# Kernel optimization log

Measured on AMD Instinct MI355X. Metric: run time of the kernel, lower is better.

The kernel has to match this reference:

```python
import jax, jax.numpy as jnp
import numpy as np

EPS = 1e-5
PATCH_LEN, STRIDE, SEQ_LEN = 16, 8, 512
D_FF, N_HEADS = 32, 8


def setup_inputs() -> dict:
    key = jax.random.key(0)
    ks = jax.random.split(key, 16)
    d_model, d_llm, V, num_tok, pred_len = 32, 4096, 32000, 1000, 96
    hf = N_HEADS * D_FF  # 256
    patch_nums = (SEQ_LEN - PATCH_LEN) // STRIDE + 2  # 64
    head_nf = D_FF * patch_nums  # 2048
    r = lambda k, s, fan: jax.random.normal(k, s, jnp.float32) / np.sqrt(fan)
    return {
        'x_enc': jax.random.normal(ks[0], (32, SEQ_LEN, 7), jnp.float32),
        'conv_w': r(ks[1], (d_model, PATCH_LEN, 3), PATCH_LEN * 3),
        'word_emb': jax.random.normal(ks[2], (V, d_llm), jnp.float32) * 0.02,
        'map_w': r(ks[3], (num_tok, V), V),
        'map_b': jnp.zeros((num_tok,), jnp.float32),
        'wq': r(ks[4], (hf, d_model), d_model), 'bq': jnp.zeros((hf,), jnp.float32),
        'wk': r(ks[5], (hf, d_llm), d_llm), 'bk': jnp.zeros((hf,), jnp.float32),
        'wv': r(ks[6], (hf, d_llm), d_llm), 'bv': jnp.zeros((hf,), jnp.float32),
        'wo': r(ks[7], (d_llm, hf), hf), 'bo': jnp.zeros((d_llm,), jnp.float32),
        'head_w': r(ks[8], (pred_len, head_nf), head_nf),
        'head_b': jnp.zeros((pred_len,), jnp.float32),
    }


def _forward(x_enc, conv_w, word_emb, map_w, map_b, wq, bq, wk, bk, wv, bv, wo, bo, head_w, head_b):
    B, T, N = x_enc.shape
    # RevIN normalize (stats detached, as in torch)
    mean = jax.lax.stop_gradient(jnp.mean(x_enc, axis=1, keepdims=True))
    stdev = jax.lax.stop_gradient(jnp.sqrt(jnp.var(x_enc, axis=1, keepdims=True) + EPS))
    x = (x_enc - mean) / stdev                      # [B,T,N]

    # Patch embedding: [B,N,T] -> replication pad -> unfold -> circular conv
    xt = jnp.transpose(x, (0, 2, 1))                # [B,N,T]
    xt = jnp.concatenate([xt, jnp.repeat(xt[..., -1:], STRIDE, axis=-1)], axis=-1)  # [B,N,T+stride]
    starts = jnp.arange(0, T + STRIDE - PATCH_LEN + 1, STRIDE)
    idx = starts[:, None] + jnp.arange(PATCH_LEN)   # [L, patch_len]
    patches = xt[:, :, idx]                         # [B,N,L,patch_len]
    L = patches.shape[2]
    p = patches.reshape(B * N, L, PATCH_LEN)
    # TokenEmbedding: conv1d over patch axis, circular pad 1, no bias
    pc = jnp.transpose(p, (0, 2, 1))                # [BN, patch_len, L]
    pc = jnp.concatenate([pc[..., -1:], pc, pc[..., :1]], axis=-1)
    emb = jax.lax.conv_general_dilated(pc, conv_w, (1,), 'VALID',
                                       dimension_numbers=('NCH', 'OIH', 'NCH'))
    enc = jnp.transpose(emb, (0, 2, 1))             # [BN, L, d_model]

    # Source embeddings: mapping_layer(word_emb.T).T -> [num_tokens, d_llm]
    src = (word_emb.T @ map_w.T + map_b).T          # [num_tok, d_llm]

    # Reprogramming cross-attention
    BN = enc.shape[0]
    q = (enc @ wq.T + bq).reshape(BN, L, N_HEADS, D_FF)   # [BN,L,H,E]
    k = (src @ wk.T + bk).reshape(-1, N_HEADS, D_FF)      # [S,H,E]
    v = (src @ wv.T + bv).reshape(-1, N_HEADS, D_FF)      # [S,H,E]
    scale = 1.0 / np.sqrt(D_FF)
    scores = jnp.einsum('blhe,she->bhls', q, k)
    A = jax.nn.softmax(scale * scores, axis=-1)
    rep = jnp.einsum('bhls,she->blhe', A, v).reshape(BN, L, N_HEADS * D_FF)
    out = rep @ wo.T + bo                           # [BN, L, d_llm]

    # LLM stubbed as identity; keep first d_ff channels (Time-LLM post-LLM path)
    dec = out[..., :D_FF]                           # [BN, L, d_ff]
    dec = dec.reshape(B, N, L, D_FF).transpose(0, 1, 3, 2)  # [B,N,d_ff,L]
    dec = dec.reshape(B, N, D_FF * L)               # FlattenHead
    dec = dec @ head_w.T + head_b                   # [B,N,pred_len]
    dec = jnp.transpose(dec, (0, 2, 1))             # [B,pred_len,N]
    # RevIN denormalize
    return dec * stdev + mean


def reference(x_enc, conv_w, word_emb, map_w, map_b, wq, bq, wk, bk, wv, bv, wo, bo, head_w, head_b):
    return _forward(x_enc, conv_w, word_emb, map_w, map_b, wq, bq, wk, bk, wv, bv, wo, bo, head_w, head_b)
```

## Files before the change

kernel.cpp:

```cpp
#include <hip/hip_runtime.h>
#include <math.h>

constexpr int B_ = 32, T_ = 512, N_ = 7, BN_ = 224;
constexpr int L_ = 64, DM_ = 32, PLEN_ = 16;
constexpr int HF_ = 256, NH_ = 8, DFF_ = 32;
constexpr int S_ = 1000, SP_ = 1024, DLLM_ = 4096, V_ = 32000;
constexpr int PRED_ = 96, HNF_ = 2048;
constexpr int KSPLIT2 = 25, KCH2 = 1280;

typedef short bf16x8 __attribute__((ext_vector_type(8)));
typedef float f32x4 __attribute__((ext_vector_type(4)));

__device__ inline ushort f2bf(float x) {
    union { float f; uint u; } v; v.f = x;
    uint r = v.u + 0x7fffu + ((v.u >> 16) & 1u);
    return (ushort)(r >> 16);
}
__device__ inline uint pk(float a, float b) {
    return (uint)f2bf(a) | ((uint)f2bf(b) << 16);
}
__device__ inline void gl16(const void* g, void* l) {
    __builtin_amdgcn_global_load_lds(
        (const __attribute__((address_space(1))) void*)g,
        (__attribute__((address_space(3))) void*)l, 16, 0, 0);
}

__global__ __launch_bounds__(256) void k_pre(const float* __restrict__ x,
                                             const float* __restrict__ conv_w,
                                             const float* __restrict__ wq,
                                             const float* __restrict__ bq,
                                             float* __restrict__ mean_o,
                                             float* __restrict__ std_o,
                                             float* __restrict__ qo) {
    const int bn = blockIdx.x, b = bn / N_, n = bn % N_;
    __shared__ float xn[520];
    __shared__ float cw[DM_ * PLEN_ * 3];
    __shared__ float enc_s[2048];
    __shared__ float wqs[HF_ * DM_];
    __shared__ float rs[4], rq[4], sm2[2];
    const int tid = threadIdx.x;
    const float* xp = x + (size_t)b * T_ * N_ + n;

    float s = 0.f, sq = 0.f;
    for (int t = tid; t < T_; t += 256) { float v = xp[(size_t)t * N_]; s += v; sq += v * v; }
    for (int i = tid; i < DM_ * PLEN_ * 3; i += 256) cw[i] = conv_w[i];
    for (int i = tid; i < HF_ * DM_; i += 256) wqs[i] = wq[i];
    for (int o = 32; o > 0; o >>= 1) { s += __shfl_down(s, o, 64); sq += __shfl_down(sq, o, 64); }
    int wid = tid >> 6, lane = tid & 63;
    if (lane == 0) { rs[wid] = s; rq[wid] = sq; }
    __syncthreads();
    if (tid == 0) {
        float S = rs[0] + rs[1] + rs[2] + rs[3];
        float Q = rq[0] + rq[1] + rq[2] + rq[3];
        float m = S / T_;
        float var = Q / T_ - m * m;
        float sd = sqrtf(var + 1e-5f);
        mean_o[bn] = m; std_o[bn] = sd;
        sm2[0] = m; sm2[1] = sd;
    }
    __syncthreads();
    const float m = sm2[0], rstd = 1.0f / sm2[1];
    for (int t = tid; t < T_; t += 256) xn[t] = (xp[(size_t)t * N_] - m) * rstd;
    __syncthreads();
    if (tid < 8) xn[T_ + tid] = xn[T_ - 1];
    __syncthreads();
    for (int idx = tid; idx < L_ * DM_ * 8; idx += 256) { }
    for (int idx = tid; idx < L_ * DM_; idx += 256) {
        int l = idx >> 5, o = idx & 31;
        float acc = 0.f;
        #pragma unroll
        for (int t = 0; t < 3; t++) {
            int col = l + t;
            int pcol = (col == 0) ? 63 : ((col == 65) ? 0 : col - 1);
            const float* xb = &xn[pcol * 8];
            const float* cwb = &cw[o * 48 + t];
            #pragma unroll
            for (int i = 0; i < 16; i++) acc += xb[i] * cwb[i * 3];
        }
        enc_s[idx] = acc;
    }
    __syncthreads();
    const float scale = 0.17677669529663687f;
    for (int idx = tid; idx < L_ * HF_; idx += 256) {
        int l = idx >> 8, c = idx & 255;
        float acc = bq[c];
        const float* e = &enc_s[l * 32];
        const float* w = &wqs[c * 32];
        #pragma unroll
        for (int k = 0; k < 32; k++) acc += e[k] * w[k];
        qo[(size_t)bn * L_ * HF_ + idx] = acc * scale;
    }
}

__global__ __launch_bounds__(256) void k_wsum(const float* __restrict__ wk,
                                              const float* __restrict__ wv,
                                              float* __restrict__ wsum) {
    int c = blockIdx.x;
    const float* row = (c < HF_) ? wk + (size_t)c * DLLM_ : wv + (size_t)(c - HF_) * DLLM_;
    float s = 0.f;
    for (int d = threadIdx.x; d < DLLM_; d += 256) s += row[d];
    for (int o = 32; o > 0; o >>= 1) s += __shfl_down(s, o, 64);
    __shared__ float rs[4];
    int wid = threadIdx.x >> 6, lane = threadIdx.x & 63;
    if (lane == 0) rs[wid] = s;
    __syncthreads();
    if (threadIdx.x == 0) wsum[c] = rs[0] + rs[1] + rs[2] + rs[3];
}

__global__ __launch_bounds__(256) void k_cvt_wkv(const float* __restrict__ wk,
                                                 const float* __restrict__ wv,
                                                 ushort* __restrict__ out) {
    int g = blockIdx.x * 256 + threadIdx.x;
    int e = g * 8;
    const float* src = (e < HF_ * DLLM_) ? wk + e : wv + (e - HF_ * DLLM_);
    float4 x = *(const float4*)src, y = *(const float4*)(src + 4);
    uint4 w; w.x = pk(x.x, x.y); w.y = pk(x.z, x.w); w.z = pk(y.x, y.y); w.w = pk(y.z, y.w);
    *(uint4*)(out + e) = w;
}

__global__ __launch_bounds__(512) void k_gemm1(const float* __restrict__ A,
                                               const ushort* __restrict__ Bw,
                                               ushort* __restrict__ ET) {
    __shared__ union {
        struct { float Af[2][128 * 32]; ushort Bs[2][256 * 32]; } st;
        ushort C[256 * 72];
    } lds;
    const int tid = threadIdx.x;
    const int lane = tid & 63, wid = tid >> 6;
    const int wr = wid >> 2, wc = wid & 3;
    const int n0 = blockIdx.x * 256, m0 = blockIdx.y * 128;

    const int arw = tid >> 3, acq = (tid & 7) ^ ((tid >> 3) & 7);
    const float* asrc0 = A + (size_t)(m0 + arw) * DLLM_ + acq * 4;
    const float* asrc1 = asrc0 + (size_t)64 * DLLM_;

    const int u0 = tid, rb0 = u0 >> 2, ob0 = (u0 & 3) ^ ((rb0 >> 1) & 3);
    const int u1 = tid + 512, rb1 = u1 >> 2, ob1 = (u1 & 3) ^ ((rb1 >> 1) & 3);
    const ushort* bptr0 = Bw + (size_t)(n0 + rb0) * DLLM_ + ob0 * 8;
    const ushort* bptr1 = Bw + (size_t)(n0 + rb1) * DLLM_ + ob1 * 8;

    const int rl = lane & 15, g = lane >> 4;
    const int oc = g ^ ((rl >> 1) & 3);

    f32x4 acc[4][4];
    #pragma unroll
    for (int i = 0; i < 4; i++)
        #pragma unroll
        for (int j = 0; j < 4; j++) acc[i][j] = (f32x4){0.f, 0.f, 0.f, 0.f};

    gl16(asrc0, &lds.st.Af[0][tid * 4]);
    gl16(asrc1, &lds.st.Af[0][(tid + 512) * 4]);
    gl16(bptr0, &lds.st.Bs[0][u0 * 8]);
    gl16(bptr1, &lds.st.Bs[0][u1 * 8]);
    __syncthreads();

    int cur = 0;
    constexpr int NT = DLLM_ / 32;
    for (int t = 0; t < NT; ++t) {
        if (t + 1 < NT) {
            const int o = (t + 1) * 32;
            gl16(asrc0 + o, &lds.st.Af[cur ^ 1][tid * 4]);
            gl16(asrc1 + o, &lds.st.Af[cur ^ 1][(tid + 512) * 4]);
            gl16(bptr0 + o, &lds.st.Bs[cur ^ 1][u0 * 8]);
            gl16(bptr1 + o, &lds.st.Bs[cur ^ 1][u1 * 8]);
            asm volatile("s_waitcnt vmcnt(4)" ::: "memory");
        } else {
            asm volatile("s_waitcnt vmcnt(0)" ::: "memory");
        }
        __builtin_amdgcn_s_barrier();
        asm volatile("" ::: "memory");
        const float* Ab = lds.st.Af[cur];
        const ushort* Bb = lds.st.Bs[cur];
        bf16x8 af[4], bfr[4];
        #pragma unroll
        for (int mi = 0; mi < 4; mi++) {
            int row = wr * 64 + mi * 16 + rl;
            int s = row & 7;
            int ulo = row * 8 + ((2 * g) ^ s);
            int uhi = row * 8 + ((2 * g + 1) ^ s);
            f32x4 xlo = *(const f32x4*)&Ab[ulo * 4];
            f32x4 xhi = *(const f32x4*)&Ab[uhi * 4];
            uint4 w; w.x = pk(xlo[0], xlo[1]); w.y = pk(xlo[2], xlo[3]);
            w.z = pk(xhi[0], xhi[1]); w.w = pk(xhi[2], xhi[3]);
            union { uint4 u; bf16x8 b; } cv; cv.u = w;
            af[mi] = cv.b;
        }
        #pragma unroll
        for (int ni = 0; ni < 4; ni++)
            bfr[ni] = *(const bf16x8*)&Bb[(wc * 64 + ni * 16 + rl) * 32 + oc * 8];
        __builtin_amdgcn_s_setprio(1);
        #pragma unroll
        for (int mi = 0; mi < 4; mi++)
            #pragma unroll
            for (int ni = 0; ni < 4; ni++)
                acc[mi][ni] = __builtin_amdgcn_mfma_f32_16x16x32_bf16(af[mi], bfr[ni], acc[mi][ni], 0, 0, 0);
        __builtin_amdgcn_s_setprio(0);
        asm volatile("s_waitcnt lgkmcnt(0)" ::: "memory");
        __builtin_amdgcn_s_barrier();
        cur ^= 1;
    }

    #pragma unroll
    for (int p = 0; p < 2; p++) {
        __syncthreads();
        if (wr == p) {
            #pragma unroll
            for (int mi = 0; mi < 4; mi++)
                #pragma unroll
                for (int ni = 0; ni < 4; ni++) {
                    int nl = wc * 64 + ni * 16 + (lane & 15);
                    int ml = mi * 16 + (lane >> 4) * 4;
                    uint2 w2;
                    w2.x = pk(acc[mi][ni][0], acc[mi][ni][1]);
                    w2.y = pk(acc[mi][ni][2], acc[mi][ni][3]);
                    *(uint2*)&lds.C[nl * 72 + ml] = w2;
                }
        }
        __syncthreads();
        {
            int r = tid >> 1, half = tid & 1;
            const uint4* src = (const uint4*)&lds.C[r * 72 + half * 32];
            ushort* dst = ET + (size_t)(n0 + r) * V_ + m0 + p * 64 + half * 32;
            uint4 v0 = src[0], v1 = src[1], v2 = src[2], v3 = src[3];
            *(uint4*)(dst + 0) = v0; *(uint4*)(dst + 8) = v1;
            *(uint4*)(dst + 16) = v2; *(uint4*)(dst + 24) = v3;
        }
    }
}

__global__ __launch_bounds__(256) void k_gemm2(const float* __restrict__ A,
                                               const ushort* __restrict__ ET,
                                               float* __restrict__ Cp) {
    __shared__ float Af[2][128 * 32];
    __shared__ ushort Bs[2][128 * 32];
    const int tid = threadIdx.x, lane = tid & 63, wid = tid >> 6;
    const int wr = wid >> 1, wc = wid & 1;
    const int m0 = blockIdx.x * 128, n0 = blockIdx.y * 128, kz = blockIdx.z;
    const size_t kbase = (size_t)kz * KCH2;

    const float* asrc[4];
    #pragma unroll
    for (int i = 0; i < 4; i++) {
        int u = i * 256 + tid;
        int r = u >> 3, c = (u & 7) ^ (r & 7);
        int rm = m0 + r; if (rm > S_ - 1) rm = S_ - 1;
        asrc[i] = A + (size_t)rm * V_ + kbase + c * 4;
    }
    const int u0 = tid, rb0 = u0 >> 2, ob0 = (u0 & 3) ^ ((rb0 >> 1) & 3);
    const int u1 = tid + 256, rb1 = u1 >> 2, ob1 = (u1 & 3) ^ ((rb1 >> 1) & 3);
    const ushort* bp0 = ET + (size_t)(n0 + rb0) * V_ + kbase + ob0 * 8;
    const ushort* bp1 = ET + (size_t)(n0 + rb1) * V_ + kbase + ob1 * 8;

    const int rl = lane & 15, g = lane >> 4;
    const int oB = g ^ ((rl >> 1) & 3);

    f32x4 acc[4][4];
    #pragma unroll
    for (int i = 0; i < 4; i++)
        #pragma unroll
        for (int j = 0; j < 4; j++) acc[i][j] = (f32x4){0.f, 0.f, 0.f, 0.f};

    gl16(bp0, &Bs[0][u0 * 8]);
    gl16(bp1, &Bs[0][u1 * 8]);
    #pragma unroll
    for (int i = 0; i < 4; i++) gl16(asrc[i], &Af[0][(i * 256 + tid) * 4]);
    __syncthreads();

    int cur = 0;
    constexpr int NT = KCH2 / 32;
    for (int t = 0; t < NT; ++t) {
        if (t + 1 < NT) {
            const int o = (t + 1) * 32;
            gl16(bp0 + o, &Bs[cur ^ 1][u0 * 8]);
            gl16(bp1 + o, &Bs[cur ^ 1][u1 * 8]);
            #pragma unroll
            for (int i = 0; i < 4; i++) gl16(asrc[i] + o, &Af[cur ^ 1][(i * 256 + tid) * 4]);
            asm volatile("s_waitcnt vmcnt(6)" ::: "memory");
        } else {
            asm volatile("s_waitcnt vmcnt(0)" ::: "memory");
        }
        __builtin_amdgcn_s_barrier();
        asm volatile("" ::: "memory");
        const float* Ab = Af[cur];
        const ushort* Bb = Bs[cur];
        bf16x8 af[4], bfr[4];
        #pragma unroll
        for (int mi = 0; mi < 4; mi++) {
            int row = wr * 64 + mi * 16 + rl;
            int s = row & 7;
            int ulo = row * 8 + ((2 * g) ^ s);
            int uhi = row * 8 + ((2 * g + 1) ^ s);
            f32x4 xlo = *(const f32x4*)&Ab[ulo * 4];
            f32x4 xhi = *(const f32x4*)&Ab[uhi * 4];
            uint4 w; w.x = pk(xlo[0], xlo[1]); w.y = pk(xlo[2], xlo[3]);
            w.z = pk(xhi[0], xhi[1]); w.w = pk(xhi[2], xhi[3]);
            union { uint4 u; bf16x8 b; } cv; cv.u = w;
            af[mi] = cv.b;
        }
        #pragma unroll
        for (int ni = 0; ni < 4; ni++)
            bfr[ni] = *(const bf16x8*)&Bb[(wc * 64 + ni * 16 + rl) * 32 + oB * 8];
        __builtin_amdgcn_s_setprio(1);
        #pragma unroll
        for (int mi = 0; mi < 4; mi++)
            #pragma unroll
            for (int ni = 0; ni < 4; ni++)
                acc[mi][ni] = __builtin_amdgcn_mfma_f32_16x16x32_bf16(af[mi], bfr[ni], acc[mi][ni], 0, 0, 0);
        __builtin_amdgcn_s_setprio(0);
        asm volatile("s_waitcnt lgkmcnt(0)" ::: "memory");
        __builtin_amdgcn_s_barrier();
        cur ^= 1;
    }

    #pragma unroll
    for (int mi = 0; mi < 4; mi++)
        #pragma unroll
        for (int ni = 0; ni < 4; ni++)
            #pragma unroll
            for (int j = 0; j < 4; j++) {
                int m = m0 + wr * 64 + mi * 16 + (lane >> 4) * 4 + j;
                int n = n0 + wc * 64 + ni * 16 + (lane & 15);
                if (m < S_) Cp[((size_t)kz * S_ + m) * 512 + n] = acc[mi][ni][j];
            }
}

__global__ __launch_bounds__(256) void k_red(const float* __restrict__ Cp,
                                             const float* __restrict__ mb,
                                             const float* __restrict__ wsum,
                                             const float* __restrict__ bk,
                                             const float* __restrict__ bv,
                                             ushort* __restrict__ Kb,
                                             ushort* __restrict__ Vt) {
    int idx = blockIdx.x * 256 + threadIdx.x;
    if (idx >= SP_ * 512) return;
    int m = idx >> 9, n = idx & 511;
    float s = 0.f;
    if (m < S_) {
        #pragma unroll
        for (int z = 0; z < KSPLIT2; z++) s += Cp[(size_t)z * S_ * 512 + (size_t)m * 512 + n];
        float bias = (n < HF_) ? bk[n] : bv[n - HF_];
        s += mb[m] * wsum[n] + bias;
    }
    ushort h = f2bf(s);
    if (n < HF_) Kb[(size_t)m * HF_ + n] = h;
    else Vt[(size_t)(n - HF_) * SP_ + m] = h;
}

__global__ __launch_bounds__(256) void k_attn(const float* __restrict__ q,
                                              const ushort* __restrict__ Kb,
                                              const ushort* __restrict__ Vt,
                                              float* __restrict__ rep) {
    const int h = blockIdx.x, bn = blockIdx.y;
    __shared__ ushort Ks[2][64 * 32];
    __shared__ ushort Vs[2][32 * 64];
    __shared__ float  Ps[4][16 * 64];
    const int tid = threadIdx.x, lane = tid & 63, w = tid >> 6;
    const int rl = lane & 15, g = lane >> 4;

    const int krow = tid >> 2, koc = (tid & 3) ^ ((krow >> 1) & 3);
    const ushort* ksrc = Kb + (size_t)krow * HF_ + h * 32 + koc * 8;
    const int verow = tid >> 3, vso = (tid & 7) ^ (verow & 7);
    const ushort* vsrc = Vt + (size_t)(h * 32 + verow) * SP_ + vso * 8;

    bf16x8 qf;
    {
        const float* qp = q + ((size_t)bn * L_ + w * 16 + rl) * HF_ + h * 32 + g * 8;
        float4 x = *(const float4*)qp, y = *(const float4*)(qp + 4);
        uint4 u; u.x = pk(x.x, x.y); u.y = pk(x.z, x.w); u.z = pk(y.x, y.y); u.w = pk(y.z, y.w);
        union { uint4 u4; bf16x8 b; } cv; cv.u4 = u; qf = cv.b;
    }

    float mrow[4] = {-1e30f, -1e30f, -1e30f, -1e30f};
    float rsum[4] = {0.f, 0.f, 0.f, 0.f};
    f32x4 oacc[2] = {(f32x4){0,0,0,0}, (f32x4){0,0,0,0}};
    float* Pw = Ps[w];

    gl16(ksrc, &Ks[0][tid * 8]);
    gl16(vsrc, &Vs[0][tid * 8]);
    __syncthreads();

    int cur = 0;
    for (int t = 0; t < 16; ++t) {
        if (t + 1 < 16) {
            gl16(ksrc + (size_t)(t + 1) * 64 * HF_, &Ks[cur ^ 1][tid * 8]);
            gl16(vsrc + (t + 1) * 64, &Vs[cur ^ 1][tid * 8]);
            asm volatile("s_waitcnt vmcnt(2)" ::: "memory");
        } else {
            asm volatile("s_waitcnt vmcnt(0)" ::: "memory");
        }
        __builtin_amdgcn_s_barrier();
        asm volatile("" ::: "memory");
        const int s0 = t * 64;

        f32x4 sc[4];
        __builtin_amdgcn_s_setprio(1);
        #pragma unroll
        for (int nf = 0; nf < 4; nf++) {
            const int row = nf * 16 + rl;
            bf16x8 kf = *(const bf16x8*)&Ks[cur][(row * 4 + (g ^ ((rl >> 1) & 3))) * 8];
            sc[nf] = __builtin_amdgcn_mfma_f32_16x16x32_bf16(qf, kf, (f32x4){0, 0, 0, 0}, 0, 0, 0);
            if (s0 + row >= S_) sc[nf] = (f32x4){-1e30f, -1e30f, -1e30f, -1e30f};
        }
        __builtin_amdgcn_s_setprio(0);
        float tmax[4];
        #pragma unroll
        for (int j = 0; j < 4; j++)
            tmax[j] = fmaxf(fmaxf(sc[0][j], sc[1][j]), fmaxf(sc[2][j], sc[3][j]));
        #pragma unroll
        for (int d = 1; d < 16; d <<= 1)
            #pragma unroll
            for (int j = 0; j < 4; j++) tmax[j] = fmaxf(tmax[j], __shfl_xor(tmax[j], d, 64));
        float resc[4];
        #pragma unroll
        for (int j = 0; j < 4; j++) {
            float mn = fmaxf(mrow[j], tmax[j]);
            resc[j] = __expf(mrow[j] - mn);
            mrow[j] = mn;
            rsum[j] *= resc[j];
            oacc[0][j] *= resc[j];
            oacc[1][j] *= resc[j];
        }
        #pragma unroll
        for (int nf = 0; nf < 4; nf++) {
            const int s = nf * 16 + rl;
            #pragma unroll
            for (int j = 0; j < 4; j++) {
                float p = __expf(sc[nf][j] - mrow[j]);
                float pf = __uint_as_float(((uint)f2bf(p)) << 16);
                rsum[j] += pf;
                const int row = 4 * g + j;
                Pw[row * 64 + (((s >> 2) ^ row) << 2) + (s & 3)] = pf;
            }
        }
        __builtin_amdgcn_s_setprio(1);
        #pragma unroll
        for (int h2 = 0; h2 < 2; h2++) {
            const int q1 = (h2 * 8 + 2 * g) ^ rl;
            const int q2 = (h2 * 8 + 2 * g + 1) ^ rl;
            f32x4 plo = *(const f32x4*)&Pw[rl * 64 + q1 * 4];
            f32x4 phi = *(const f32x4*)&Pw[rl * 64 + q2 * 4];
            uint4 pu; pu.x = pk(plo[0], plo[1]); pu.y = pk(plo[2], plo[3]);
            pu.z = pk(phi[0], phi[1]); pu.w = pk(phi[2], phi[3]);
            union { uint4 u; bf16x8 b; } cv; cv.u = pu;
            bf16x8 pa = cv.b;
            #pragma unroll
            for (int eg = 0; eg < 2; eg++) {
                const int erow = eg * 16 + rl;
                const int su = (h2 * 4 + g) ^ (erow & 7);
                bf16x8 vf = *(const bf16x8*)&Vs[cur][erow * 64 + su * 8];
                oacc[eg] = __builtin_amdgcn_mfma_f32_16x16x32_bf16(pa, vf, oacc[eg], 0, 0, 0);
            }
        }
        __builtin_amdgcn_s_setprio(0);
        asm volatile("s_waitcnt lgkmcnt(0)" ::: "memory");
        __builtin_amdgcn_s_barrier();
        cur ^= 1;
    }

    #pragma unroll
    for (int d = 1; d < 16; d <<= 1)
        #pragma unroll
        for (int j = 0; j < 4; j++) rsum[j] += __shfl_xor(rsum[j], d, 64);
    float inv[4];
    #pragma unroll
    for (int j = 0; j < 4; j++) inv[j] = 1.0f / rsum[j];
    #pragma unroll
    for (int eg = 0; eg < 2; eg++)
        #pragma unroll
        for (int j = 0; j < 4; j++)
            rep[((size_t)bn * HF_ + h * 32 + eg * 16 + rl) * 64 + w * 16 + 4 * g + j] =
                oacc[eg][j] * inv[j];
}

__global__ __launch_bounds__(256) void k_post(const float* __restrict__ rep,
                                              const float* __restrict__ wo,
                                              const float* __restrict__ bo,
                                              const float* __restrict__ hw,
                                              const float* __restrict__ hb,
                                              const float* __restrict__ mean_i,
                                              const float* __restrict__ std_i,
                                              float* __restrict__ out) {
    const int bn = blockIdx.x, b = bn / N_, n = bn % N_;
    __shared__ float woT[HF_ * 32];
    __shared__ float dt[2048];
    const int tid = threadIdx.x;
    for (int idx = tid; idx < HF_ * 32; idx += 256) {
        int e = idx & 31, c = idx >> 5;
        woT[c * 32 + e] = wo[(size_t)e * HF_ + c];
    }
    __syncthreads();
    {
        const int l = tid & 63, e0 = (tid >> 6) * 8;
        float acc[8];
        #pragma unroll
        for (int i = 0; i < 8; i++) acc[i] = bo[e0 + i];
        const float* rp = rep + (size_t)bn * HF_ * 64 + l;
        for (int c = 0; c < HF_; c++) {
            float rv = rp[(size_t)c * 64];
            #pragma unroll
            for (int i = 0; i < 8; i++) acc[i] += rv * woT[c * 32 + e0 + i];
        }
        #pragma unroll
        for (int i = 0; i < 8; i++) dt[l * 32 + e0 + i] = acc[i];
    }
    __syncthreads();
    const float m = mean_i[bn], sd = std_i[bn];
    for (int p = tid; p < PRED_; p += 256) {
        float acc = hb[p];
        const float* w = hw + (size_t)p * HNF_;
        for (int f = 0; f < DFF_; f++) {
            const float* wf = w + f * 64;
            #pragma unroll
            for (int ll = 0; ll < 64; ll++) acc += dt[ll * 32 + f] * wf[ll];
        }
        out[(size_t)b * PRED_ * N_ + (size_t)p * N_ + n] = acc * sd + m;
    }
}

extern "C" void kernel_launch(void* const* d_in, const int* in_sizes, int n_in,
                              void* d_out, int out_size, void* d_ws, size_t ws_size,
                              hipStream_t stream) {
    const float* x_enc   = (const float*)d_in[0];
    const float* conv_w  = (const float*)d_in[1];
    const float* word_emb= (const float*)d_in[2];
    const float* map_w   = (const float*)d_in[3];
    const float* map_b   = (const float*)d_in[4];
    const float* wq      = (const float*)d_in[5];
    const float* bq      = (const float*)d_in[6];
    const float* wk      = (const float*)d_in[7];
    const float* bk      = (const float*)d_in[8];
    const float* wv      = (const float*)d_in[9];
    const float* bv      = (const float*)d_in[10];
    const float* wo      = (const float*)d_in[11];
    const float* bo      = (const float*)d_in[12];
    const float* head_w  = (const float*)d_in[13];
    const float* head_b  = (const float*)d_in[14];

    float* ws = (float*)d_ws;
    float* mean_w = ws;
    float* std_w  = ws + 256;
    float* wsum_w = ws + 512;
    float* q_w    = ws + 1024;
    float* kv_w   = q_w + (size_t)BN_ * L_ * HF_;
    float* cp_w   = kv_w + (size_t)S_ * 512;
    float* rep_w  = cp_w;
    ushort* et_w  = (ushort*)(cp_w + (size_t)KSPLIT2 * S_ * 512);
    ushort* wkv_w = et_w + (size_t)512 * V_;
    ushort* kb_w  = (ushort*)kv_w;
    ushort* vt_w  = kb_w + (size_t)SP_ * HF_;

    k_pre<<<BN_, 256, 0, stream>>>(x_enc, conv_w, wq, bq, mean_w, std_w, q_w);
    k_wsum<<<512, 256, 0, stream>>>(wk, wv, wsum_w);
    k_cvt_wkv<<<(512 * DLLM_ / 8) / 256, 256, 0, stream>>>(wk, wv, wkv_w);
    k_gemm1<<<dim3(2, V_ / 128), 512, 0, stream>>>(word_emb, wkv_w, et_w);
    k_gemm2<<<dim3(8, 4, KSPLIT2), 256, 0, stream>>>(map_w, et_w, cp_w);
    k_red<<<(SP_ * 512) / 256, 256, 0, stream>>>(cp_w, map_b, wsum_w, bk, bv, kb_w, vt_w);
    k_attn<<<dim3(NH_, BN_), 256, 0, stream>>>(q_w, kb_w, vt_w, rep_w);
    k_post<<<BN_, 256, 0, stream>>>(rep_w, wo, bo, head_w, head_b, mean_w, std_w, (float*)d_out);
}
```

Measured before the change: 555.2 us.

## Fuse weight sum with bf16 conversion, shrink gemm1 tile, drop attention double buffering

The separate wk/wv row-sum and bf16 conversion kernels become one kernel that reads each weight row once, removing one launch and one pass over the weights. gemm1 moves from 128x256 tiles with 512 threads to 128x128 tiles with 256 threads, which doubles the grid and halves LDS per block. That gives more blocks per CU but means the fp32 A tile is reloaded for twice as many column blocks. The attention kernel drops its double-buffered K/V prefetch and instead loads synchronously with __syncthreads, which cuts LDS use but exposes load latency.

After: 701.2 us. 1.26x slower.

```diff
diff --git a/kernel.cpp b/kernel.cpp
--- a/kernel.cpp
+++ b/kernel.cpp
@@ -64,7 +64,6 @@
     __syncthreads();
     if (tid < 8) xn[T_ + tid] = xn[T_ - 1];
     __syncthreads();
-    for (int idx = tid; idx < L_ * DM_ * 8; idx += 256) { }
     for (int idx = tid; idx < L_ * DM_; idx += 256) {
         int l = idx >> 5, o = idx & 31;
         float acc = 0.f;
@@ -92,55 +91,55 @@
     }
 }
 
-__global__ __launch_bounds__(256) void k_wsum(const float* __restrict__ wk,
+__global__ __launch_bounds__(256) void k_cvtw(const float* __restrict__ wk,
                                               const float* __restrict__ wv,
+                                              ushort* __restrict__ out,
                                               float* __restrict__ wsum) {
-    int c = blockIdx.x;
+    const int c = blockIdx.x, tid = threadIdx.x;
     const float* row = (c < HF_) ? wk + (size_t)c * DLLM_ : wv + (size_t)(c - HF_) * DLLM_;
+    const float* p = row + tid * 16;
+    ushort* o = out + (size_t)c * DLLM_ + tid * 16;
     float s = 0.f;
-    for (int d = threadIdx.x; d < DLLM_; d += 256) s += row[d];
-    for (int o = 32; o > 0; o >>= 1) s += __shfl_down(s, o, 64);
+    #pragma unroll
+    for (int i = 0; i < 4; i++) {
+        float4 x = *(const float4*)(p + i * 4);
+        s += x.x + x.y + x.z + x.w;
+        uint2 w; w.x = pk(x.x, x.y); w.y = pk(x.z, x.w);
+        *(uint2*)(o + i * 4) = w;
+    }
+    for (int off = 32; off > 0; off >>= 1) s += __shfl_down(s, off, 64);
     __shared__ float rs[4];
-    int wid = threadIdx.x >> 6, lane = threadIdx.x & 63;
+    int wid = tid >> 6, lane = tid & 63;
     if (lane == 0) rs[wid] = s;
     __syncthreads();
-    if (threadIdx.x == 0) wsum[c] = rs[0] + rs[1] + rs[2] + rs[3];
-}
-
-__global__ __launch_bounds__(256) void k_cvt_wkv(const float* __restrict__ wk,
-                                                 const float* __restrict__ wv,
-                                                 ushort* __restrict__ out) {
-    int g = blockIdx.x * 256 + threadIdx.x;
-    int e = g * 8;
-    const float* src = (e < HF_ * DLLM_) ? wk + e : wv + (e - HF_ * DLLM_);
-    float4 x = *(const float4*)src, y = *(const float4*)(src + 4);
-    uint4 w; w.x = pk(x.x, x.y); w.y = pk(x.z, x.w); w.z = pk(y.x, y.y); w.w = pk(y.z, y.w);
-    *(uint4*)(out + e) = w;
-}
-
-__global__ __launch_bounds__(512) void k_gemm1(const float* __restrict__ A,
+    if (tid == 0) wsum[c] = rs[0] + rs[1] + rs[2] + rs[3];
+}
+
+__global__ __launch_bounds__(256) void k_gemm1(const float* __restrict__ A,
                                                const ushort* __restrict__ Bw,
                                                ushort* __restrict__ ET) {
     __shared__ union {
-        struct { float Af[2][128 * 32]; ushort Bs[2][256 * 32]; } st;
-        ushort C[256 * 72];
+        struct { float Af[2][128 * 32]; ushort Bs[2][128 * 32]; } st;
+        ushort C[128 * 72];
     } lds;
-    const int tid = threadIdx.x;
-    const int lane = tid & 63, wid = tid >> 6;
-    const int wr = wid >> 2, wc = wid & 3;
-    const int n0 = blockIdx.x * 256, m0 = blockIdx.y * 128;
-
-    const int arw = tid >> 3, acq = (tid & 7) ^ ((tid >> 3) & 7);
-    const float* asrc0 = A + (size_t)(m0 + arw) * DLLM_ + acq * 4;
-    const float* asrc1 = asrc0 + (size_t)64 * DLLM_;
-
+    const int tid = threadIdx.x, lane = tid & 63, wid = tid >> 6;
+    const int wr = wid >> 1, wc = wid & 1;
+    const int n0 = blockIdx.x * 128, m0 = blockIdx.y * 128;
+
+    const float* asrc[4];
+    #pragma unroll
+    for (int i = 0; i < 4; i++) {
+        int u = i * 256 + tid;
+        int r = u >> 3, c = (u & 7) ^ (r & 7);
+        asrc[i] = A + (size_t)(m0 + r) * DLLM_ + c * 4;
+    }
     const int u0 = tid, rb0 = u0 >> 2, ob0 = (u0 & 3) ^ ((rb0 >> 1) & 3);
-    const int u1 = tid + 512, rb1 = u1 >> 2, ob1 = (u1 & 3) ^ ((rb1 >> 1) & 3);
-    const ushort* bptr0 = Bw + (size_t)(n0 + rb0) * DLLM_ + ob0 * 8;
-    const ushort* bptr1 = Bw + (size_t)(n0 + rb1) * DLLM_ + ob1 * 8;
+    const int u1 = tid + 256, rb1 = u1 >> 2, ob1 = (u1 & 3) ^ ((rb1 >> 1) & 3);
+    const ushort* bp0 = Bw + (size_t)(n0 + rb0) * DLLM_ + ob0 * 8;
+    const ushort* bp1 = Bw + (size_t)(n0 + rb1) * DLLM_ + ob1 * 8;
 
     const int rl = lane & 15, g = lane >> 4;
-    const int oc = g ^ ((rl >> 1) & 3);
+    const int oB = g ^ ((rl >> 1) & 3);
 
     f32x4 acc[4][4];
     #pragma unroll
@@ -148,10 +147,10 @@
         #pragma unroll
         for (int j = 0; j < 4; j++) acc[i][j] = (f32x4){0.f, 0.f, 0.f, 0.f};
 
-    gl16(asrc0, &lds.st.Af[0][tid * 4]);
-    gl16(asrc1, &lds.st.Af[0][(tid + 512) * 4]);
-    gl16(bptr0, &lds.st.Bs[0][u0 * 8]);
-    gl16(bptr1, &lds.st.Bs[0][u1 * 8]);
+    gl16(bp0, &lds.st.Bs[0][u0 * 8]);
+    gl16(bp1, &lds.st.Bs[0][u1 * 8]);
+    #pragma unroll
+    for (int i = 0; i < 4; i++) gl16(asrc[i], &lds.st.Af[0][(i * 256 + tid) * 4]);
     __syncthreads();
 
     int cur = 0;
@@ -159,11 +158,11 @@
     for (int t = 0; t < NT; ++t) {
         if (t + 1 < NT) {
             const int o = (t + 1) * 32;
-            gl16(asrc0 + o, &lds.st.Af[cur ^ 1][tid * 4]);
-            gl16(asrc1 + o, &lds.st.Af[cur ^ 1][(tid + 512) * 4]);
-            gl16(bptr0 + o, &lds.st.Bs[cur ^ 1][u0 * 8]);
-            gl16(bptr1 + o, &lds.st.Bs[cur ^ 1][u1 * 8]);
-            asm volatile("s_waitcnt vmcnt(4)" ::: "memory");
+            gl16(bp0 + o, &lds.st.Bs[cur ^ 1][u0 * 8]);
+            gl16(bp1 + o, &lds.st.Bs[cur ^ 1][u1 * 8]);
+            #pragma unroll
+            for (int i = 0; i < 4; i++) gl16(asrc[i] + o, &lds.st.Af[cur ^ 1][(i * 256 + tid) * 4]);
+            asm volatile("s_waitcnt vmcnt(6)" ::: "memory");
         } else {
             asm volatile("s_waitcnt vmcnt(0)" ::: "memory");
         }
@@ -187,7 +186,7 @@
         }
         #pragma unroll
         for (int ni = 0; ni < 4; ni++)
-            bfr[ni] = *(const bf16x8*)&Bb[(wc * 64 + ni * 16 + rl) * 32 + oc * 8];
+            bfr[ni] = *(const bf16x8*)&Bb[(wc * 64 + ni * 16 + rl) * 32 + oB * 8];
         __builtin_amdgcn_s_setprio(1);
         #pragma unroll
         for (int mi = 0; mi < 4; mi++)
@@ -351,16 +350,18 @@
                                               const ushort* __restrict__ Vt,
                                               float* __restrict__ rep) {
     const int h = blockIdx.x, bn = blockIdx.y;
-    __shared__ ushort Ks[2][64 * 32];
-    __shared__ ushort Vs[2][32 * 64];
+    __shared__ ushort Ks[64 * 32];
+    __shared__ ushort Vs[32 * 64];
     __shared__ float  Ps[4][16 * 64];
     const int tid = threadIdx.x, lane = tid & 63, w = tid >> 6;
     const int rl = lane & 15, g = lane >> 4;
 
     const int krow = tid >> 2, koc = (tid & 3) ^ ((krow >> 1) & 3);
     const ushort* ksrc = Kb + (size_t)krow * HF_ + h * 32 + koc * 8;
+    ushort* kdst = &Ks[tid * 8];
     const int verow = tid >> 3, vso = (tid & 7) ^ (verow & 7);
     const ushort* vsrc = Vt + (size_t)(h * 32 + verow) * SP_ + vso * 8;
+    ushort* vdst = &Vs[tid * 8];
 
     bf16x8 qf;
     {
@@ -375,29 +376,18 @@
     f32x4 oacc[2] = {(f32x4){0,0,0,0}, (f32x4){0,0,0,0}};
     float* Pw = Ps[w];
 
-    gl16(ksrc, &Ks[0][tid * 8]);
-    gl16(vsrc, &Vs[0][tid * 8]);
-    __syncthreads();
-
-    int cur = 0;
     for (int t = 0; t < 16; ++t) {
-        if (t + 1 < 16) {
-            gl16(ksrc + (size_t)(t + 1) * 64 * HF_, &Ks[cur ^ 1][tid * 8]);
-            gl16(vsrc + (t + 1) * 64, &Vs[cur ^ 1][tid * 8]);
-            asm volatile("s_waitcnt vmcnt(2)" ::: "memory");
-        } else {
-            asm volatile("s_waitcnt vmcnt(0)" ::: "memory");
-        }
-        __builtin_amdgcn_s_barrier();
-        asm volatile("" ::: "memory");
         const int s0 = t * 64;
+        gl16(ksrc + (size_t)s0 * HF_, kdst);
+        gl16(vsrc + s0, vdst);
+        __syncthreads();
 
         f32x4 sc[4];
         __builtin_amdgcn_s_setprio(1);
         #pragma unroll
         for (int nf = 0; nf < 4; nf++) {
             const int row = nf * 16 + rl;
-            bf16x8 kf = *(const bf16x8*)&Ks[cur][(row * 4 + (g ^ ((rl >> 1) & 3))) * 8];
+            bf16x8 kf = *(const bf16x8*)&Ks[(row * 4 + (g ^ ((rl >> 1) & 3))) * 8];
             sc[nf] = __builtin_amdgcn_mfma_f32_16x16x32_bf16(qf, kf, (f32x4){0, 0, 0, 0}, 0, 0, 0);
             if (s0 + row >= S_) sc[nf] = (f32x4){-1e30f, -1e30f, -1e30f, -1e30f};
         }
@@ -447,14 +437,12 @@
             for (int eg = 0; eg < 2; eg++) {
                 const int erow = eg * 16 + rl;
                 const int su = (h2 * 4 + g) ^ (erow & 7);
-                bf16x8 vf = *(const bf16x8*)&Vs[cur][erow * 64 + su * 8];
+                bf16x8 vf = *(const bf16x8*)&Vs[erow * 64 + su * 8];
                 oacc[eg] = __builtin_amdgcn_mfma_f32_16x16x32_bf16(pa, vf, oacc[eg], 0, 0, 0);
             }
         }
         __builtin_amdgcn_s_setprio(0);
-        asm volatile("s_waitcnt lgkmcnt(0)" ::: "memory");
-        __builtin_amdgcn_s_barrier();
-        cur ^= 1;
+        __syncthreads();
     }
 
     #pragma unroll
@@ -550,9 +538,8 @@
     ushort* vt_w  = kb_w + (size_t)SP_ * HF_;
 
     k_pre<<<BN_, 256, 0, stream>>>(x_enc, conv_w, wq, bq, mean_w, std_w, q_w);
-    k_wsum<<<512, 256, 0, stream>>>(wk, wv, wsum_w);
-    k_cvt_wkv<<<(512 * DLLM_ / 8) / 256, 256, 0, stream>>>(wk, wv, wkv_w);
-    k_gemm1<<<dim3(2, V_ / 128), 512, 0, stream>>>(word_emb, wkv_w, et_w);
+    k_cvtw<<<512, 256, 0, stream>>>(wk, wv, wkv_w, wsum_w);
+    k_gemm1<<<dim3(4, V_ / 128), 256, 0, stream>>>(word_emb, wkv_w, et_w);
     k_gemm2<<<dim3(8, 4, KSPLIT2), 256, 0, stream>>>(map_w, et_w, cp_w);
     k_red<<<(SP_ * 512) / 256, 256, 0, stream>>>(cp_w, map_b, wsum_w, bk, bv, kb_w, vt_w);
     k_attn<<<dim3(NH_, BN_), 256, 0, stream>>>(q_w, kb_w, vt_w, rep_w);
```
